# Kernel optimization log

Hardware: AMD Instinct MI355X
Metric: run time of the kernel (lower is better)

## Reference

```python
import jax, jax.numpy as jnp
import numpy as np

N_HEAD = 16
WINDOW = 256


def setup_inputs() -> dict:
    key = jax.random.key(0)
    ks = jax.random.split(key, 3)
    B, S, D = 2, 2048, 1024
    x = jax.random.normal(ks[0], (B, S, D), dtype=jnp.float32)
    w_attn = jax.random.normal(ks[1], (D, 3 * D), dtype=jnp.float32) * 0.02
    b_attn = jnp.zeros((3 * D,), dtype=jnp.float32)
    w_proj = jax.random.normal(ks[2], (D, D), dtype=jnp.float32) * 0.02
    b_proj = jnp.zeros((D,), dtype=jnp.float32)
    return {"x": x, "w_attn": w_attn, "b_attn": b_attn, "w_proj": w_proj, "b_proj": b_proj}


def reference(x, w_attn, b_attn, w_proj, b_proj):
    B, S, D = x.shape
    hd = D // N_HEAD  # head dim
    scale = 1.0 / np.sqrt(hd).astype(np.float32)

    # fused QKV projection (Conv1D == linear on last dim)
    c = jnp.einsum('bsd,df->bsf', x, w_attn) + b_attn
    q, k, v = jnp.split(c, 3, axis=-1)

    def split_heads(t):  # [B,S,D] -> [B,H,S,hd]
        return t.reshape(B, S, N_HEAD, hd).transpose(0, 2, 1, 3)

    q, k, v = split_heads(q), split_heads(k), split_heads(v)
    present = jnp.stack([k, v], axis=1)  # [B,2,H,S,hd]

    # scores [B,H,S,S]
    w = jnp.einsum('bhqd,bhkd->bhqk', q, k) * scale

    # causal sliding-window mask
    q_pos = jnp.arange(S)[:, None]
    k_pos = jnp.arange(S)[None, :]
    mask = (k_pos <= q_pos) & (k_pos >= q_pos - WINDOW + 1)  # [S,S]
    w = jnp.where(mask[None, None], w, jnp.finfo(w.dtype).min)
    w = jax.nn.softmax(w, axis=-1)

    a = jnp.einsum('bhqk,bhkd->bhqd', w, v)
    a = a.transpose(0, 2, 1, 3).reshape(B, S, D)  # merge heads
    out = jnp.einsum('bsd,df->bsf', a, w_proj) + b_proj
    return out, present
```

## Files before the change

kernel.cpp:

```cpp
#include <hip/hip_runtime.h>
#include <cstdint>
#include <cstddef>

typedef __bf16 bf16x8 __attribute__((ext_vector_type(8)));
typedef float f32x4 __attribute__((ext_vector_type(4)));

#define MFMA16(a, b, c) __builtin_amdgcn_mfma_f32_16x16x32_bf16(a, b, c, 0, 0, 0)

static __device__ __forceinline__ bf16x8 ld_bf16x8(const __bf16* p) {
    return *reinterpret_cast<const bf16x8*>(p);
}

static __device__ __forceinline__ void async_cp16(const __bf16* g, __bf16* l) {
    __builtin_amdgcn_global_load_lds((const __attribute__((address_space(1))) void*)g,
                                     (__attribute__((address_space(3))) void*)l, 16, 0, 0);
}

template <int N>
static __device__ __forceinline__ void wait_vmcnt() {
    asm volatile("s_waitcnt vmcnt(%0)" ::"n"(N) : "memory");
}

static __device__ __forceinline__ void barrier_pinned() {
    __builtin_amdgcn_sched_barrier(0);
    __builtin_amdgcn_s_barrier();
    __builtin_amdgcn_sched_barrier(0);
}

template <int CTRL>
static __device__ __forceinline__ float dppmv(float x) {
    return __builtin_bit_cast(float, __builtin_amdgcn_update_dpp(
        0, __builtin_bit_cast(int, x), CTRL, 0xF, 0xF, true));
}
static __device__ __forceinline__ float rmax16(float x) {
    x = fmaxf(x, dppmv<0x121>(x));
    x = fmaxf(x, dppmv<0x122>(x));
    x = fmaxf(x, dppmv<0x124>(x));
    x = fmaxf(x, dppmv<0x128>(x));
    return x;
}
static __device__ __forceinline__ float rsum16(float x) {
    x += dppmv<0x121>(x);
    x += dppmv<0x122>(x);
    x += dppmv<0x124>(x);
    x += dppmv<0x128>(x);
    return x;
}

__global__ void cvt_kernel(const float* __restrict__ src, __bf16* __restrict__ dst, int n8) {
    int i = blockIdx.x * blockDim.x + threadIdx.x;
    if (i >= n8) return;
    const float4* s4 = reinterpret_cast<const float4*>(src) + (size_t)i * 2;
    float4 a = s4[0], b = s4[1];
    bf16x8 o;
    o[0] = (__bf16)a.x; o[1] = (__bf16)a.y; o[2] = (__bf16)a.z; o[3] = (__bf16)a.w;
    o[4] = (__bf16)b.x; o[5] = (__bf16)b.y; o[6] = (__bf16)b.z; o[7] = (__bf16)b.w;
    reinterpret_cast<bf16x8*>(dst)[i] = o;
}

__global__ __launch_bounds__(256) void tcvt_kernel(const float* __restrict__ in,
                                                   __bf16* __restrict__ out, int K, int N) {
    __shared__ __bf16 T[64][72];
    const int k0 = blockIdx.y * 64, n0 = blockIdx.x * 64;
    const int t = threadIdx.x;
    const int col = (t & 15) << 2;
    const int rowb = t >> 4;
    #pragma unroll
    for (int i = 0; i < 4; i++) {
        int row = i * 16 + rowb;
        float4 v = *reinterpret_cast<const float4*>(&in[(size_t)(k0 + row) * N + n0 + col]);
        T[col + 0][row] = (__bf16)v.x;
        T[col + 1][row] = (__bf16)v.y;
        T[col + 2][row] = (__bf16)v.z;
        T[col + 3][row] = (__bf16)v.w;
    }
    __syncthreads();
    const int oc = (t & 7) << 3;
    const int orb = t >> 3;
    #pragma unroll
    for (int i = 0; i < 2; i++) {
        int r = i * 32 + orb;
        bf16x8 v = *reinterpret_cast<bf16x8*>(&T[r][oc]);
        *reinterpret_cast<bf16x8*>(&out[(size_t)(n0 + r) * K + k0 + oc]) = v;
    }
}

template <int BM, int BN, int WM, int WN>
__device__ __forceinline__ void mainloop2(const __bf16* __restrict__ A,
                                          const __bf16* __restrict__ Bt,
                                          int K, int row0, int col0,
                                          __bf16* lds,
                                          f32x4 (&acc)[BM / WM / 16][BN / WN / 16]) {
    constexpr int MR = BM / WM / 16, NR = BN / WN / 16;
    constexpr int AE = BM * 32;
    constexpr int BUFE = AE + BN * 32;
    constexpr int APW = BM / 16 / 8;
    constexpr int BPW = BN / 16 / 8;
    const int tid = threadIdx.x, l = tid & 63, w = tid >> 6;
    const int wm = w / WN, wn = w % WN;
    const int lr = l >> 2;
    const int lcs = (((l & 3) ^ ((l >> 3) & 3)) << 3);
    const int fr = l & 15;
    const int fc = (((l >> 4) ^ ((l >> 1) & 3)) << 3);

    const size_t arow = (size_t)(row0 + lr) * K + lcs;
    const size_t brow = (size_t)(col0 + lr) * K + lcs;
    const int nt = K >> 5;

    auto stage = [&](int t, int buf) {
        const int k0 = t << 5;
        const int bb = buf * BUFE;
        #pragma unroll
        for (int j = 0; j < APW; j++) {
            const int mi = w * APW + j;
            async_cp16(A + arow + (size_t)mi * 16 * K + k0, lds + bb + mi * 512 + l * 8);
        }
        #pragma unroll
        for (int j = 0; j < BPW; j++) {
            const int ni = w * BPW + j;
            async_cp16(Bt + brow + (size_t)ni * 16 * K + k0, lds + bb + AE + ni * 512 + l * 8);
        }
    };

    stage(0, 0);
    stage(1, 1);

    const int aoff = (wm * (BM / WM) + fr) * 32 + fc;
    const int boff = AE + (wn * (BN / WN) + fr) * 32 + fc;

    int p = 0;
    for (int t = 0; t < nt; ++t) {
        if (t + 1 < nt) {
            wait_vmcnt<APW + BPW>();
        } else {
            wait_vmcnt<0>();
        }
        barrier_pinned();
        if (t + 2 < nt) {
            int p2 = p + 2; if (p2 >= 3) p2 -= 3;
            stage(t + 2, p2);
        }
        const int cb = p * BUFE;
        bf16x8 af[MR], bfv[NR];
        #pragma unroll
        for (int m = 0; m < MR; m++) af[m] = ld_bf16x8(&lds[cb + aoff + m * 512]);
        #pragma unroll
        for (int n = 0; n < NR; n++) bfv[n] = ld_bf16x8(&lds[cb + boff + n * 512]);
        __builtin_amdgcn_s_setprio(1);
        #pragma unroll
        for (int m = 0; m < MR; m++) {
            #pragma unroll
            for (int n = 0; n < NR; n++) {
                acc[m][n] = MFMA16(af[m], bfv[n], acc[m][n]);
            }
        }
        __builtin_amdgcn_s_setprio(0);
        asm volatile("s_waitcnt lgkmcnt(0)" ::: "memory");
        __builtin_amdgcn_sched_barrier(0);
        p = (p == 2) ? 0 : p + 1;
    }
}

__global__ __launch_bounds__(512, 2) void gemm_qkv_kernel(const __bf16* __restrict__ xb,
                                                          const __bf16* __restrict__ wabt,
                                                          const float* __restrict__ bias,
                                                          __bf16* __restrict__ qb,
                                                          __bf16* __restrict__ kb,
                                                          __bf16* __restrict__ vt,
                                                          float* __restrict__ present) {
    __shared__ __bf16 lds[3 * (128 * 32 + 128 * 32)];
    f32x4 acc[2][4] = {};
    const int row0 = blockIdx.y * 128, col0 = blockIdx.x * 128;
    mainloop2<128, 128, 4, 2>(xb, wabt, 1024, row0, col0, lds, acc);

    const int l = threadIdx.x & 63, w = threadIdx.x >> 6;
    const int wm = w >> 1, wn = w & 1;
    const int part = col0 >> 10;
    #pragma unroll
    for (int n = 0; n < 4; n++) {
        int col = col0 + wn * 64 + n * 16 + (l & 15);
        int hh = (col >> 6) & 15;
        int dd = col & 63;
        float bv = bias[col];
        #pragma unroll
        for (int m = 0; m < 2; m++) {
            #pragma unroll
            for (int r = 0; r < 4; r++) {
                int row = row0 + wm * 32 + m * 16 + ((l >> 4) << 2) + r;
                int bb = row >> 11, ss = row & 2047;
                float val = acc[m][n][r] + bv;
                size_t qi = (((size_t)(bb * 16 + hh)) * 2048 + ss) * 64 + dd;
                if (part == 0) {
                    qb[qi] = (__bf16)val;
                } else if (part == 1) {
                    kb[qi] = (__bf16)val;
                    present[(((size_t)((bb * 2 + 0) * 16 + hh)) * 2048 + ss) * 64 + dd] = val;
                } else {
                    vt[(((size_t)(bb * 16 + hh)) * 64 + dd) * 2048 + ss] = (__bf16)val;
                    present[(((size_t)((bb * 2 + 1) * 16 + hh)) * 2048 + ss) * 64 + dd] = val;
                }
            }
        }
    }
}

__global__ __launch_bounds__(512, 2) void gemm_proj_kernel(const __bf16* __restrict__ ab,
                                                           const __bf16* __restrict__ wpbt,
                                                           const float* __restrict__ bias,
                                                           float* __restrict__ out) {
    __shared__ __bf16 lds[3 * (128 * 32 + 128 * 32)];
    f32x4 acc[2][4] = {};
    const int row0 = blockIdx.y * 128, col0 = blockIdx.x * 128;
    mainloop2<128, 128, 4, 2>(ab, wpbt, 1024, row0, col0, lds, acc);

    const int lane = threadIdx.x & 63, w = threadIdx.x >> 6;
    const int wm = w >> 1, wn = w & 1;
    #pragma unroll
    for (int n = 0; n < 4; n++) {
        int col = col0 + wn * 64 + n * 16 + (lane & 15);
        float bv = bias[col];
        #pragma unroll
        for (int m = 0; m < 2; m++) {
            #pragma unroll
            for (int r = 0; r < 4; r++) {
                int row = row0 + wm * 32 + m * 16 + ((lane >> 4) << 2) + r;
                out[(size_t)row * 1024 + col] = acc[m][n][r] + bv;
            }
        }
    }
}

__global__ __launch_bounds__(256) void attn_kernel(const __bf16* __restrict__ qb,
                                                   const __bf16* __restrict__ kb,
                                                   const __bf16* __restrict__ vtb,
                                                   __bf16* __restrict__ ab) {
    __shared__ __bf16 Pls[4][16 * 40];
    const int bh = blockIdx.x >> 5;
    const int qt = blockIdx.x & 31;
    const int lane = threadIdx.x & 63, wid = threadIdx.x >> 6;
    const int q0w = qt * 64 + wid * 16;

    const __bf16* Qh = qb + (size_t)bh * 2048 * 64;
    const __bf16* Kh = kb + (size_t)bh * 2048 * 64;
    const __bf16* Vt = vtb + (size_t)bh * 64 * 2048;
    __bf16* Pw = &Pls[wid][0];

    bf16x8 qf[2];
    {
        int qr = q0w + (lane & 15);
        const __bf16* qp = Qh + (size_t)qr * 64 + ((lane >> 4) << 3);
        qf[0] = ld_bf16x8(qp);
        qf[1] = ld_bf16x8(qp + 32);
    }

    f32x4 o[4];
    #pragma unroll
    for (int dt = 0; dt < 4; dt++) o[dt] = (f32x4){0.f, 0.f, 0.f, 0.f};
    float mrun[4] = {-1e30f, -1e30f, -1e30f, -1e30f};
    float srun[4] = {0.f, 0.f, 0.f, 0.f};

    const float cl2 = 0.18033688f;
    int klo = q0w - 255;
    int kt0 = klo > 0 ? (klo & ~31) : 0;

    for (int kt = kt0; kt <= q0w + 15; kt += 32) {
        bf16x8 vf[4];
        #pragma unroll
        for (int dt = 0; dt < 4; dt++)
            vf[dt] = ld_bf16x8(&Vt[(size_t)(dt * 16 + (lane & 15)) * 2048 + kt + ((lane >> 4) << 3)]);
        f32x4 s[2];
        #pragma unroll
        for (int kc = 0; kc < 2; kc++) {
            int krow = kt + kc * 16 + (lane & 15);
            const __bf16* kp = Kh + (size_t)krow * 64 + ((lane >> 4) << 3);
            bf16x8 kf0 = ld_bf16x8(kp);
            bf16x8 kf1 = ld_bf16x8(kp + 32);
            f32x4 a = (f32x4){0.f, 0.f, 0.f, 0.f};
            a = MFMA16(qf[0], kf0, a);
            a = MFMA16(qf[1], kf1, a);
            s[kc] = a;
        }
        const bool clean = (kt >= q0w - 240) && (kt + 31 <= q0w);
        float p0v[4], p1v[4];
        if (clean) {
            float s0v[4], s1v[4], mx[4];
            #pragma unroll
            for (int r = 0; r < 4; r++) {
                s0v[r] = s[0][r] * cl2;
                s1v[r] = s[1][r] * cl2;
                mx[r] = rmax16(fmaxf(s0v[r], s1v[r]));
            }
            float grow = fmaxf(fmaxf(mx[0] - mrun[0], mx[1] - mrun[1]),
                               fmaxf(mx[2] - mrun[2], mx[3] - mrun[3]));
            if (__all(grow <= 8.f)) {
                #pragma unroll
                for (int r = 0; r < 4; r++) {
                    float p0 = exp2f(s0v[r] - mrun[r]);
                    float p1 = exp2f(s1v[r] - mrun[r]);
                    srun[r] += rsum16(p0 + p1);
                    p0v[r] = p0;
                    p1v[r] = p1;
                }
            } else {
                float factor[4];
                #pragma unroll
                for (int r = 0; r < 4; r++) {
                    float mn = fmaxf(mrun[r], mx[r]);
                    float f = exp2f(mrun[r] - mn);
                    float p0 = exp2f(s0v[r] - mn);
                    float p1 = exp2f(s1v[r] - mn);
                    srun[r] = srun[r] * f + rsum16(p0 + p1);
                    mrun[r] = mn;
                    factor[r] = f;
                    p0v[r] = p0;
                    p1v[r] = p1;
                }
                #pragma unroll
                for (int dt = 0; dt < 4; dt++) {
                    #pragma unroll
                    for (int r = 0; r < 4; r++) o[dt][r] *= factor[r];
                }
            }
        } else {
            float factor[4];
            #pragma unroll
            for (int r = 0; r < 4; r++) {
                int q = q0w + ((lane >> 4) << 2) + r;
                int k0i = kt + (lane & 15);
                int k1i = k0i + 16;
                bool ok0 = (k0i <= q) && (k0i > q - 256);
                bool ok1 = (k1i <= q) && (k1i > q - 256);
                float s0 = ok0 ? s[0][r] * cl2 : -1e30f;
                float s1 = ok1 ? s[1][r] * cl2 : -1e30f;
                float mx = rmax16(fmaxf(s0, s1));
                float mn = fmaxf(mrun[r], mx);
                float f = exp2f(mrun[r] - mn);
                float p0 = ok0 ? exp2f(s0 - mn) : 0.f;
                float p1 = ok1 ? exp2f(s1 - mn) : 0.f;
                srun[r] = srun[r] * f + rsum16(p0 + p1);
                mrun[r] = mn;
                factor[r] = f;
                p0v[r] = p0;
                p1v[r] = p1;
            }
            #pragma unroll
            for (int dt = 0; dt < 4; dt++) {
                #pragma unroll
                for (int r = 0; r < 4; r++) o[dt][r] *= factor[r];
            }
        }
        #pragma unroll
        for (int r = 0; r < 4; r++) {
            int qrow = ((lane >> 4) << 2) + r;
            Pw[qrow * 40 + (lane & 15)] = (__bf16)p0v[r];
            Pw[qrow * 40 + 16 + (lane & 15)] = (__bf16)p1v[r];
        }
        asm volatile("s_waitcnt lgkmcnt(0)" ::: "memory");
        bf16x8 pf = ld_bf16x8(&Pw[(lane & 15) * 40 + ((lane >> 4) << 3)]);
        #pragma unroll
        for (int dt = 0; dt < 4; dt++) {
            o[dt] = MFMA16(pf, vf[dt], o[dt]);
        }
    }

    const int bb = bh >> 4, hh = bh & 15;
    #pragma unroll
    for (int r = 0; r < 4; r++) {
        int q = q0w + ((lane >> 4) << 2) + r;
        float inv = 1.f / srun[r];
        size_t base = ((size_t)bb * 2048 + q) * 1024 + hh * 64;
        #pragma unroll
        for (int dt = 0; dt < 4; dt++) {
            ab[base + dt * 16 + (lane & 15)] = (__bf16)(o[dt][r] * inv);
        }
    }
}

extern "C" void kernel_launch(void* const* d_in, const int* in_sizes, int n_in,
                              void* d_out, int out_size, void* d_ws, size_t ws_size,
                              hipStream_t stream) {
    const float* x = (const float*)d_in[0];
    const float* w_attn = (const float*)d_in[1];
    const float* b_attn = (const float*)d_in[2];
    const float* w_proj = (const float*)d_in[3];
    const float* b_proj = (const float*)d_in[4];

    float* out = (float*)d_out;
    float* present = out + (size_t)2 * 2048 * 1024;

    char* w = (char*)d_ws;
    __bf16* xb   = (__bf16*)(w);
    __bf16* wabt = (__bf16*)(w + 8388608);
    __bf16* wpbt = (__bf16*)(w + 14680064);
    __bf16* qb   = (__bf16*)(w + 16777216);
    __bf16* kb   = (__bf16*)(w + 25165824);
    __bf16* vt   = (__bf16*)(w + 33554432);
    __bf16* ab   = xb;

    cvt_kernel<<<2048, 256, 0, stream>>>(x, xb, 524288);
    tcvt_kernel<<<dim3(48, 16), 256, 0, stream>>>(w_attn, wabt, 1024, 3072);
    tcvt_kernel<<<dim3(16, 16), 256, 0, stream>>>(w_proj, wpbt, 1024, 1024);

    gemm_qkv_kernel<<<dim3(24, 32), 512, 0, stream>>>(xb, wabt, b_attn, qb, kb, vt, present);

    attn_kernel<<<1024, 256, 0, stream>>>(qb, kb, vt, ab);

    gemm_proj_kernel<<<dim3(8, 32), 512, 0, stream>>>(ab, wpbt, b_proj, out);
}
```

Measured before the change: 123.0 us.

## Prefetch next K/V tiles in registers, remap blocks per XCD, add setprio

The attention kernel now loads the next 32-key tile of K and V^T into registers while computing on the current one, so global-load latency overlaps the MFMA and softmax work. Block indices are remapped so that the four heads handled by one XCD share its L2 cache. s_setprio raises wave priority around the MFMA sections. The cost is extra VGPRs for the double-buffered fragments, which can lower occupancy.

```diff
diff --git a/kernel.cpp b/kernel.cpp
--- a/kernel.cpp
+++ b/kernel.cpp
@@ -235,8 +235,10 @@
                                                    const __bf16* __restrict__ vtb,
                                                    __bf16* __restrict__ ab) {
     __shared__ __bf16 Pls[4][16 * 40];
-    const int bh = blockIdx.x >> 5;
-    const int qt = blockIdx.x & 31;
+    const int bidx = blockIdx.x;
+    const int xcd = bidx & 7, idx = bidx >> 3;
+    const int bh = (xcd << 2) | (idx & 3);
+    const int qt = idx >> 2;
     const int lane = threadIdx.x & 63, wid = threadIdx.x >> 6;
     const int q0w = qt * 64 + wid * 16;
 
@@ -245,10 +247,11 @@
     const __bf16* Vt = vtb + (size_t)bh * 64 * 2048;
     __bf16* Pw = &Pls[wid][0];
 
+    const int ld16 = lane & 15, hi3 = (lane >> 4) << 3;
+
     bf16x8 qf[2];
     {
-        int qr = q0w + (lane & 15);
-        const __bf16* qp = Qh + (size_t)qr * 64 + ((lane >> 4) << 3);
+        const __bf16* qp = Qh + (size_t)(q0w + ld16) * 64 + hi3;
         qf[0] = ld_bf16x8(qp);
         qf[1] = ld_bf16x8(qp + 32);
     }
@@ -262,24 +265,51 @@
     const float cl2 = 0.18033688f;
     int klo = q0w - 255;
     int kt0 = klo > 0 ? (klo & ~31) : 0;
-
-    for (int kt = kt0; kt <= q0w + 15; kt += 32) {
-        bf16x8 vf[4];
-        #pragma unroll
-        for (int dt = 0; dt < 4; dt++)
-            vf[dt] = ld_bf16x8(&Vt[(size_t)(dt * 16 + (lane & 15)) * 2048 + kt + ((lane >> 4) << 3)]);
+    const int ktend = q0w + 15;
+
+    bf16x8 k0a, k0b, k1a, k1b, v0, v1, v2, v3;
+    {
+        const __bf16* kp = Kh + (size_t)(kt0 + ld16) * 64 + hi3;
+        k0a = ld_bf16x8(kp);
+        k0b = ld_bf16x8(kp + 32);
+        k1a = ld_bf16x8(kp + 1024);
+        k1b = ld_bf16x8(kp + 1024 + 32);
+        v0 = ld_bf16x8(&Vt[(size_t)(ld16) * 2048 + kt0 + hi3]);
+        v1 = ld_bf16x8(&Vt[(size_t)(16 + ld16) * 2048 + kt0 + hi3]);
+        v2 = ld_bf16x8(&Vt[(size_t)(32 + ld16) * 2048 + kt0 + hi3]);
+        v3 = ld_bf16x8(&Vt[(size_t)(48 + ld16) * 2048 + kt0 + hi3]);
+    }
+
+    for (int kt = kt0; kt <= ktend; kt += 32) {
+        const bool more = (kt + 32) <= ktend;
+        bf16x8 nk0a, nk0b, nk1a, nk1b, nv0, nv1, nv2, nv3;
+        if (more) {
+            const int ktn = kt + 32;
+            const __bf16* kp = Kh + (size_t)(ktn + ld16) * 64 + hi3;
+            nk0a = ld_bf16x8(kp);
+            nk0b = ld_bf16x8(kp + 32);
+            nk1a = ld_bf16x8(kp + 1024);
+            nk1b = ld_bf16x8(kp + 1024 + 32);
+            nv0 = ld_bf16x8(&Vt[(size_t)(ld16) * 2048 + ktn + hi3]);
+            nv1 = ld_bf16x8(&Vt[(size_t)(16 + ld16) * 2048 + ktn + hi3]);
+            nv2 = ld_bf16x8(&Vt[(size_t)(32 + ld16) * 2048 + ktn + hi3]);
+            nv3 = ld_bf16x8(&Vt[(size_t)(48 + ld16) * 2048 + ktn + hi3]);
+        }
         f32x4 s[2];
-        #pragma unroll
-        for (int kc = 0; kc < 2; kc++) {
-            int krow = kt + kc * 16 + (lane & 15);
-            const __bf16* kp = Kh + (size_t)krow * 64 + ((lane >> 4) << 3);
-            bf16x8 kf0 = ld_bf16x8(kp);
-            bf16x8 kf1 = ld_bf16x8(kp + 32);
+        __builtin_amdgcn_s_setprio(1);
+        {
             f32x4 a = (f32x4){0.f, 0.f, 0.f, 0.f};
-            a = MFMA16(qf[0], kf0, a);
-            a = MFMA16(qf[1], kf1, a);
-            s[kc] = a;
-        }
+            a = MFMA16(qf[0], k0a, a);
+            a = MFMA16(qf[1], k0b, a);
+            s[0] = a;
+        }
+        {
+            f32x4 a = (f32x4){0.f, 0.f, 0.f, 0.f};
+            a = MFMA16(qf[0], k1a, a);
+            a = MFMA16(qf[1], k1b, a);
+            s[1] = a;
+        }
+        __builtin_amdgcn_s_setprio(0);
         const bool clean = (kt >= q0w - 240) && (kt + 31 <= q0w);
         float p0v[4], p1v[4];
         if (clean) {
@@ -326,7 +356,7 @@
             #pragma unroll
             for (int r = 0; r < 4; r++) {
                 int q = q0w + ((lane >> 4) << 2) + r;
-                int k0i = kt + (lane & 15);
+                int k0i = kt + ld16;
                 int k1i = k0i + 16;
                 bool ok0 = (k0i <= q) && (k0i > q - 256);
                 bool ok1 = (k1i <= q) && (k1i > q - 256);
@@ -352,14 +382,20 @@
         #pragma unroll
         for (int r = 0; r < 4; r++) {
             int qrow = ((lane >> 4) << 2) + r;
-            Pw[qrow * 40 + (lane & 15)] = (__bf16)p0v[r];
-            Pw[qrow * 40 + 16 + (lane & 15)] = (__bf16)p1v[r];
+            Pw[qrow * 40 + ld16] = (__bf16)p0v[r];
+            Pw[qrow * 40 + 16 + ld16] = (__bf16)p1v[r];
         }
         asm volatile("s_waitcnt lgkmcnt(0)" ::: "memory");
-        bf16x8 pf = ld_bf16x8(&Pw[(lane & 15) * 40 + ((lane >> 4) << 3)]);
-        #pragma unroll
-        for (int dt = 0; dt < 4; dt++) {
-            o[dt] = MFMA16(pf, vf[dt], o[dt]);
+        bf16x8 pf = ld_bf16x8(&Pw[ld16 * 40 + hi3]);
+        __builtin_amdgcn_s_setprio(1);
+        o[0] = MFMA16(pf, v0, o[0]);
+        o[1] = MFMA16(pf, v1, o[1]);
+        o[2] = MFMA16(pf, v2, o[2]);
+        o[3] = MFMA16(pf, v3, o[3]);
+        __builtin_amdgcn_s_setprio(0);
+        if (more) {
+            k0a = nk0a; k0b = nk0b; k1a = nk1a; k1b = nk1b;
+            v0 = nv0; v1 = nv1; v2 = nv2; v3 = nv3;
         }
     }
 
@@ -371,7 +407,7 @@
         size_t base = ((size_t)bb * 2048 + q) * 1024 + hh * 64;
         #pragma unroll
         for (int dt = 0; dt < 4; dt++) {
-            ab[base + dt * 16 + (lane & 15)] = (__bf16)(o[dt][r] * inv);
+            ab[base + dt * 16 + ld16] = (__bf16)(o[dt][r] * inv);
         }
     }
 }
```

Measured after the change: 119.0 us. -3.3%, faster.
